# Kernel optimization log

Measured on AMD Instinct MI355X. Metric: run time of the kernel, lower is better.

## Reference

```python
import jax, jax.numpy as jnp
import numpy as np

B, C, H = 4, 64, 48
HEADS, BSWIN = 2, 4
BIG = [3, 6, 12, 24]      # big window edge per scale (cubic)
SMALL = [1, 2, 4, 8]      # small (pool) window edge per scale
NH = 3                    # small windows per big window per dim (= big/small)
L = NH ** 3               # tokens per big window after pooling
CPH = C // (HEADS * BSWIN)  # channels per head per scale = 8


def _rel_pos_index():
    coords = np.stack(np.meshgrid(*([np.arange(NH)] * 3), indexing='ij')).reshape(3, -1)
    rel = coords[:, :, None] - coords[:, None, :] + (NH - 1)
    span = 2 * NH - 1
    return jnp.asarray(rel[0] * span * span + rel[1] * span + rel[2])  # (L, L) int

REL_IDX = _rel_pos_index()


def _interp_matrix(n_in, n_out):
    # 1D linear interpolation matrix, align_corners=True (matches F.interpolate)
    if n_out == n_in:
        return jnp.eye(n_in, dtype=jnp.float32)
    pos = jnp.arange(n_out, dtype=jnp.float32) * (n_in - 1) / (n_out - 1)
    i0 = jnp.clip(jnp.floor(pos).astype(jnp.int32), 0, n_in - 2)
    w = pos - i0.astype(jnp.float32)
    r = jnp.arange(n_out)
    m = jnp.zeros((n_out, n_in), jnp.float32)
    return m.at[r, i0].add(1.0 - w).at[r, i0 + 1].add(w)


def _gather(x):
    # x: (B, C, H, H, H) -> (B, HEADS, sum_N, L, CPH)
    b = x.shape[0]
    x = x.reshape(b, BSWIN, HEADS, CPH, H, H, H)
    parts, Ns = [], []
    for i in range(BSWIN):
        bw, sw = BIG[i], SMALL[i]
        N1 = H // bw
        xi = x[:, i].reshape(b, HEADS, CPH, N1, NH, sw, N1, NH, sw, N1, NH, sw)
        xi = xi.max(axis=(5, 8, 11))  # max-pool each small window
        # (b, head, c, Nh, nh, Nw, nw, Nd, nd) -> b head (Nh Nw Nd) (nh nw nd) c
        xi = xi.transpose(0, 1, 3, 5, 7, 4, 6, 8, 2)
        parts.append(xi.reshape(b, HEADS, N1 ** 3, L, CPH))
        Ns.append(N1)
    return jnp.concatenate(parts, axis=2), Ns


def _scatter(attn, Ns):
    # attn: (B, HEADS, sum_N, L, CPH) -> (B, C, H, H, H)
    b = attn.shape[0]
    outs, idx = [], 0
    for i in range(BSWIN):
        bw, sw = BIG[i], SMALL[i]
        N1 = Ns[i]
        N = N1 ** 3
        o = attn[:, :, idx:idx + N].reshape(b, HEADS, N, NH, NH, NH, CPH)
        M = _interp_matrix(NH, bw)  # trilinear upsample by small window size
        o = jnp.einsum('bhnijkc,pi,qj,rk->bhnpqrc', o, M, M, M)
        o = o.reshape(b, HEADS, N1, N1, N1, bw, bw, bw, CPH)
        # b head Nh Nw Nd wh ww wd c -> b head c (Nh wh) (Nw ww) (Nd wd)
        o = o.transpose(0, 1, 8, 2, 5, 3, 6, 4, 7).reshape(b, HEADS, CPH, H, H, H)
        outs.append(o)
        idx += N
    out = jnp.stack(outs, axis=1)  # b bswin head c h w d
    return out.reshape(b, C, H, H, H)


def _attention(q, k, v, rpb_table):
    c = q.shape[-1]
    scores = jnp.einsum('bhNmc,bhNnc->bhNmn', q, k) / jnp.sqrt(jnp.asarray(c, q.dtype))
    w = jax.nn.softmax(scores, axis=-1)
    bias = rpb_table[REL_IDX].transpose(2, 0, 1)  # (head, L, L), added POST-softmax
    w = w + bias[None, :, None]
    return jnp.einsum('bhNmn,bhNnc->bhNmc', w, v)


def setup_inputs() -> dict:
    key = jax.random.key(0)
    kq, kk, kv, kp = jax.random.split(key, 4)
    shp = (B, C, H, H, H)
    return {
        'query': jax.random.normal(kq, shp, jnp.float32),
        'key': jax.random.normal(kk, shp, jnp.float32),
        'value': jax.random.normal(kv, shp, jnp.float32),
        'rpb_table': jax.random.normal(kp, ((2 * NH - 1) ** 3, HEADS), jnp.float32) * 0.02,
    }


def reference(query, key, value, rpb_table):
    q, Ns = _gather(query)
    k, _ = _gather(key)
    v, _ = _gather(value)
    attn = _attention(q, k, v, rpb_table)
    return _scatter(attn, Ns)
```

## Files before the change

kernel.cpp:

```cpp
#include <hip/hip_runtime.h>


static constexpr long S1 = 4L * 48 * 24 * 24 * 24;
static constexpr long S2 = 4L * 32 * 12 * 12 * 12;
static constexpr long S3 = 4L * 16 * 6 * 6 * 6;


__device__ __forceinline__ void pool48_body(int pid, float* xp,
                                            const float* __restrict__ q,
                                            const float* __restrict__ k,
                                            const float* __restrict__ v,
                                            float* __restrict__ P1)
{
    constexpr int RSTRIDE = 28;
    const int tz = pid % 3;
    int rest = pid / 3;
    const int zc = rest % 12; rest /= 12;
    const int c = rest % 48;
    const int b = rest / 48;

    const float* in = tz == 0 ? q : (tz == 1 ? k : v);
    float* o = P1 + (long)tz * S1;
    const float* base = in + ((long)b * 64 + 16 + c) * 110592 + (long)(zc * 4) * 2304;

    for (int i = threadIdx.x; i < 4 * 48 * 12; i += 256) {
        int p = i / 576;
        int rem = i % 576;
        int r = rem / 12;
        int x4 = rem % 12;
        float4 f = *(const float4*)(base + (long)p * 2304 + r * 48 + 4 * x4);
        float2 m = make_float2(fmaxf(f.x, f.y), fmaxf(f.z, f.w));
        *(float2*)(&xp[(p * 48 + r) * RSTRIDE + 2 * x4]) = m;
    }
    __syncthreads();

    for (int i = threadIdx.x; i < 288; i += 256) {
        int zl = i / 144;
        int rem = i % 144;
        int oy = rem / 6;
        int ox4 = rem % 6;
        const float* p0 = &xp[((2 * zl) * 48 + 2 * oy) * RSTRIDE + 4 * ox4];
        const float* p1 = p0 + RSTRIDE;
        const float* p2 = p0 + 48 * RSTRIDE;
        const float* p3 = p2 + RSTRIDE;
        float4 a = *(const float4*)p0;
        float4 bb = *(const float4*)p1;
        float4 cc = *(const float4*)p2;
        float4 d = *(const float4*)p3;
        float4 r4 = make_float4(fmaxf(fmaxf(a.x, bb.x), fmaxf(cc.x, d.x)),
                                fmaxf(fmaxf(a.y, bb.y), fmaxf(cc.y, d.y)),
                                fmaxf(fmaxf(a.z, bb.z), fmaxf(cc.z, d.z)),
                                fmaxf(fmaxf(a.w, bb.w), fmaxf(cc.w, d.w)));
        long oaddr = (((long)b * 48 + c) * 24 + (zc * 2 + zl)) * 576 + oy * 24 + 4 * ox4;
        *(float4*)(o + oaddr) = r4;
    }
}

__device__ __forceinline__ void attn0_body(int aid, float* smem,
                                           const float* __restrict__ qsrc,
                                           const float* __restrict__ ksrc,
                                           const float* __restrict__ vsrc,
                                           const float* __restrict__ rpb,
                                           float* __restrict__ out)
{
    const int half = aid & 1;
    int rest = aid >> 1;
    const int Wy = rest % 16; rest /= 16;
    const int Wz = rest % 16; rest /= 16;
    const int head = rest % 2;
    const int b = rest / 2;

    float* tile = smem;
    float* bias = smem + 5184;
    const int tid = threadIdx.x;

    for (int i = tid; i < 2 * 729; i += 256) {
        int h = i / 729;
        int mn = i % 729;
        int m = mn / 27, n = mn % 27;
        int mi = m / 9, mj = (m / 3) % 3, mk = m % 3;
        int ni = n / 9, nj = (n / 3) % 3, nk = n % 3;
        int ridx = (mi - ni + 2) * 25 + (mj - nj + 2) * 5 + (mk - nk + 2);
        bias[i] = rpb[ridx * 2 + h];
    }

    for (int i = tid; i < 1296; i += 256) {
        int seg = i / 6;
        int off = (i % 6) * 4;
        int tz = seg / 72;
        int rem = seg % 72;
        int cph = rem / 9;
        int rem2 = rem % 9;
        int zt = rem2 / 3;
        int r = rem2 % 3;
        const float* src = tz == 0 ? qsrc : (tz == 1 ? ksrc : vsrc);
        long addr = ((((long)b * 64 + head * 8 + cph) * 48 + 3 * Wz + zt) * 48
                     + 3 * Wy + r) * 48 + half * 24 + off;
        float4 f = *(const float4*)(src + addr);
        float vals[4] = {f.x, f.y, f.z, f.w};
#pragma unroll
        for (int j = 0; j < 4; j++) {
            int xl = off + j;
            int wxl = xl / 3, tk = xl % 3;
            int tok = zt * 9 + r * 3 + tk;
            tile[((wxl * 3 + tz) * 27 + tok) * 8 + cph] = vals[j];
        }
    }
    __syncthreads();

    const int wx = tid >> 5;
    const int lane = tid & 31;
    if (lane < 27) {
        const int m = lane;
        const float* tq = tile + (wx * 3 + 0) * 27 * 8;
        const float* tk = tile + (wx * 3 + 1) * 27 * 8;
        const float* tv = tile + (wx * 3 + 2) * 27 * 8;
        float qr[8];
#pragma unroll
        for (int c = 0; c < 8; c++) qr[c] = tq[m * 8 + c];

        float s[27];
        float mx = -1e30f;
#pragma unroll
        for (int n = 0; n < 27; n++) {
            float acc = 0.f;
#pragma unroll
            for (int c = 0; c < 8; c++) acc += qr[c] * tk[n * 8 + c];
            acc *= 0.35355339059327373f;
            s[n] = acc;
            mx = fmaxf(mx, acc);
        }
        float sum = 0.f;
#pragma unroll
        for (int n = 0; n < 27; n++) {
            s[n] = __expf(s[n] - mx);
            sum += s[n];
        }
        float rs = 1.0f / sum;

        float o[8] = {0, 0, 0, 0, 0, 0, 0, 0};
#pragma unroll
        for (int n = 0; n < 27; n++) {
            float wgt = s[n] * rs + bias[(head * 27 + m) * 27 + n];
#pragma unroll
            for (int c = 0; c < 8; c++) o[c] += wgt * tv[n * 8 + c];
        }
        float* to = tile + (wx * 3 + 0) * 27 * 8;
#pragma unroll
        for (int c = 0; c < 8; c++) to[m * 8 + c] = o[c];
    }
    __syncthreads();

    for (int i = tid; i < 432; i += 256) {
        int x4i = i % 6;
        int t2 = i / 6;
        int cph = t2 % 8; t2 /= 8;
        int y = t2 % 3;
        int zl = t2 / 3;
        float4 res;
        float* rr = (float*)&res;
#pragma unroll
        for (int e = 0; e < 4; e++) {
            int xl = x4i * 4 + e;
            int wxl = xl / 3, tk = xl % 3;
            int tok = zl * 9 + y * 3 + tk;
            rr[e] = tile[(wxl * 3 + 0) * 27 * 8 + tok * 8 + cph];
        }
        int z = 3 * Wz + zl;
        int Y = 3 * Wy + y;
        long oaddr = (((long)(b * 64 + head * 8 + cph) * 48 + z) * 48 + Y) * 48
                     + half * 24 + x4i * 4;
        *(float4*)(out + oaddr) = res;
    }
}

__global__ void fused_pool_attn0(const float* __restrict__ q,
                                 const float* __restrict__ k,
                                 const float* __restrict__ v,
                                 const float* __restrict__ rpb,
                                 float* __restrict__ P1,
                                 float* __restrict__ out)
{
    __shared__ float smem[6642];
    const int bx = blockIdx.x;
    if (bx < 8192 && (bx & 1) == 0) {
        attn0_body(bx >> 1, smem, q, k, v, rpb, out);
    } else {
        int pid = (bx < 8192) ? (bx >> 1) : (bx - 4096);
        pool48_body(pid, smem, q, k, v, P1);
    }
}

template <int OUTW>
__global__ void pool_kernel(const float* __restrict__ in0,
                            const float* __restrict__ in1,
                            const float* __restrict__ in2,
                            float* __restrict__ out, long outStride,
                            int Cin, int chOff, int Cout, int Din, int n)
{
    const float* in = blockIdx.y == 0 ? in0 : (blockIdx.y == 1 ? in1 : in2);
    float* o = out + (long)blockIdx.y * outStride;
    const int Dout = Din >> 1;
    const int QX = Dout / OUTW;
    int idx = blockIdx.x * blockDim.x + threadIdx.x;
    if (idx >= n) return;
    int qx = idx % QX;
    int t = idx / QX;
    int y = t % Dout; t /= Dout;
    int z = t % Dout; t /= Dout;
    int c = t % Cout;
    int b = t / Cout;
    const float* p = in + ((((long)b * Cin + c + chOff) * Din + 2 * z) * Din + 2 * y) * Din
                        + qx * (2 * OUTW);
    const float* rows[4] = { p, p + Din, p + (long)Din * Din, p + (long)Din * Din + Din };

    float v2[4][2 * OUTW];
#pragma unroll
    for (int r = 0; r < 4; r++) {
#pragma unroll
        for (int j = 0; j < OUTW / 2; j++) {
            float4 f = *(const float4*)(rows[r] + 4 * j);
            v2[r][4 * j + 0] = f.x; v2[r][4 * j + 1] = f.y;
            v2[r][4 * j + 2] = f.z; v2[r][4 * j + 3] = f.w;
        }
    }
    float res[OUTW];
#pragma unroll
    for (int i = 0; i < OUTW; i++) {
        float m0 = fmaxf(v2[0][2 * i], v2[0][2 * i + 1]);
        float m1 = fmaxf(v2[1][2 * i], v2[1][2 * i + 1]);
        float m2 = fmaxf(v2[2][2 * i], v2[2][2 * i + 1]);
        float m3 = fmaxf(v2[3][2 * i], v2[3][2 * i + 1]);
        res[i] = fmaxf(fmaxf(m0, m1), fmaxf(m2, m3));
    }
    long oaddr = ((((long)b * Cout + c) * Dout + z) * Dout + y) * Dout + qx * OUTW;
    if (OUTW == 4) {
        *(float4*)(o + oaddr) = make_float4(res[0], res[1], res[2], res[3 % OUTW]);
    } else {
        *(float2*)(o + oaddr) = make_float2(res[0], res[1]);
    }
}

template <int S>
__global__ void attn_kernel(const float* __restrict__ qsrc,
                            const float* __restrict__ ksrc,
                            const float* __restrict__ vsrc,
                            const float* __restrict__ rpb,
                            float* __restrict__ attnOut)
{
    constexpr int N1 = (S == 1 ? 8 : S == 2 ? 4 : 2);
    constexpr int D  = 3 * N1;
    constexpr int Cs = (S == 1 ? 48 : S == 2 ? 32 : 16);
    constexpr int scaleOff = (S == 1 ? 4096 : S == 2 ? 4608 : 4672);
    constexpr int VEC = (S == 3 ? 2 : 4);
    constexpr int SEG = 3 * D;
    constexpr int NSEG = 72;
    constexpr int TOTV = NSEG * SEG / VEC;

    __shared__ float tile[N1][3][27][8];
    __shared__ float bias_lds[2][27][27];

    const int b = blockIdx.z;
    const int head = blockIdx.y;
    const int Wz = blockIdx.x / N1;
    const int Wy = blockIdx.x % N1;

    for (int i = threadIdx.x; i < 2 * 729; i += blockDim.x) {
        int h = i / 729;
        int mn = i % 729;
        int m = mn / 27, n = mn % 27;
        int mi = m / 9, mj = (m / 3) % 3, mk = m % 3;
        int ni = n / 9, nj = (n / 3) % 3, nk = n % 3;
        int ridx = (mi - ni + 2) * 25 + (mj - nj + 2) * 5 + (mk - nk + 2);
        bias_lds[h][m][n] = rpb[ridx * 2 + h];
    }

    for (int i = threadIdx.x; i < TOTV; i += blockDim.x) {
        int seg = i / (SEG / VEC);
        int off = (i % (SEG / VEC)) * VEC;
        int tz = seg / 24;
        int rem = seg % 24;
        int cph = rem / 3;
        int zt = rem % 3;
        const float* src = tz == 0 ? qsrc : (tz == 1 ? ksrc : vsrc);
        long base = ((((long)b * Cs + head * 8 + cph) * D + (3 * Wz + zt)) * D + 3 * Wy) * (long)D;
        const float* sp = src + base + off;
        float vals[VEC];
        if (VEC == 4) {
            float4 f = *(const float4*)sp;
            vals[0] = f.x; vals[1] = f.y; vals[2] = f.z; vals[3 % VEC] = f.w;
        } else {
            float2 f = *(const float2*)sp;
            vals[0] = f.x; vals[1] = f.y;
        }
#pragma unroll
        for (int j = 0; j < VEC; j++) {
            int f = off + j;
            int r = f / D;
            int x = f % D;
            tile[x / 3][tz][zt * 9 + r * 3 + (x % 3)][cph] = vals[j];
        }
    }
    __syncthreads();

    const int wx = threadIdx.x >> 5;
    const int lane = threadIdx.x & 31;
    if (lane >= 27) return;
    const int m = lane;

    float qr[8];
#pragma unroll
    for (int c = 0; c < 8; c++) qr[c] = tile[wx][0][m][c];

    float s[27];
    float mx = -1e30f;
#pragma unroll
    for (int n = 0; n < 27; n++) {
        float acc = 0.f;
#pragma unroll
        for (int c = 0; c < 8; c++) acc += qr[c] * tile[wx][1][n][c];
        acc *= 0.35355339059327373f;
        s[n] = acc;
        mx = fmaxf(mx, acc);
    }
    float sum = 0.f;
#pragma unroll
    for (int n = 0; n < 27; n++) {
        s[n] = __expf(s[n] - mx);
        sum += s[n];
    }
    float rs = 1.0f / sum;

    float o[8] = {0, 0, 0, 0, 0, 0, 0, 0};
#pragma unroll
    for (int n = 0; n < 27; n++) {
        float wgt = s[n] * rs + bias_lds[head][m][n];
#pragma unroll
        for (int c = 0; c < 8; c++) o[c] += wgt * tile[wx][2][n][c];
    }

    const int win = (Wz * N1 + Wy) * N1 + wx;
    float* dst = attnOut + (((long)(b * 2 + head) * 4680 + scaleOff + win) * 27 + m) * 8;
    *(float4*)(dst) = make_float4(o[0], o[1], o[2], o[3]);
    *(float4*)(dst + 4) = make_float4(o[4], o[5], o[6], o[7]);
}

template <int S>
__device__ __forceinline__ void scatter_impl(const float* __restrict__ attn,
                                             float* __restrict__ out,
                                             float* lds, int t, int b, int head,
                                             int tid)
{
    constexpr int bw = (S == 1 ? 6 : S == 2 ? 12 : 24);
    constexpr int N1 = 48 / bw;
    constexpr int scaleOff = (S == 1 ? 4096 : S == 2 ? 4608 : 4672);
    constexpr int CZ = (S == 1 ? 3 : 1);
    constexpr int NZC = bw / CZ;
    constexpr int LDSF = N1 * 216;
    constexpr int NF4 = CZ * bw * 8 * 12;

    const int zc = t % NZC; t /= NZC;
    const int Wy = t % N1;
    const int Wz = t / N1;

    const float* src = attn + ((long)(b * 2 + head) * 4680 + scaleOff + (Wz * N1 + Wy) * N1) * 216;
    for (int i = tid; i < LDSF / 4; i += 256)
        *(float4*)(lds + 4 * i) = *(const float4*)(src + 4 * i);
    __syncthreads();

    const float inv = 2.0f / (float)(bw - 1);

    for (int i = tid; i < NF4; i += 256) {
        int x4 = i % 12;
        int t2 = i / 12;
        int cph = t2 % 8; t2 /= 8;
        int y = t2 % bw;
        int zl = t2 / bw;
        int wp = zc * CZ + zl;

        float posp = wp * inv; int i0p = min((int)posp, 1); float fp = posp - (float)i0p;
        float posq = y * inv;  int i0q = min((int)posq, 1); float fq = posq - (float)i0q;
        float wpv[2] = {1.f - fp, fp};
        float wqv[2] = {1.f - fq, fq};
        float4 res;
        float* rr = (float*)&res;
#pragma unroll
        for (int e = 0; e < 4; e++) {
            int r = x4 * 4 + e;
            int Wx = r / bw, wr = r % bw;
            float posr = wr * inv; int i0r = min((int)posr, 1); float fr = posr - (float)i0r;
            float wrv[2] = {1.f - fr, fr};
            const float* basep = lds + Wx * 216 + cph;
            float acc = 0.f;
#pragma unroll
            for (int di = 0; di < 2; di++) {
#pragma unroll
                for (int dj = 0; dj < 2; dj++) {
#pragma unroll
                    for (int dk = 0; dk < 2; dk++) {
                        int tok = ((i0p + di) * 3 + (i0q + dj)) * 3 + (i0r + dk);
                        acc += wpv[di] * wqv[dj] * wrv[dk] * basep[tok * 8];
                    }
                }
            }
            rr[e] = acc;
        }

        int z = Wz * bw + wp;
        int Y = Wy * bw + y;
        long oaddr = (((long)(b * 64 + S * 16 + head * 8 + cph) * 48 + z) * 48 + Y) * 48 + x4 * 4;
        *(float4*)(out + oaddr) = res;
    }
}

__global__ void scatter_all(const float* __restrict__ attn, float* __restrict__ out)
{
    __shared__ float lds[8 * 216];
    const int b = blockIdx.z;
    const int head = blockIdx.y;
    const int bx = blockIdx.x;
    const int tid = threadIdx.x;
    if (bx < 128)      scatter_impl<1>(attn, out, lds, bx,       b, head, tid);
    else if (bx < 320) scatter_impl<2>(attn, out, lds, bx - 128, b, head, tid);
    else               scatter_impl<3>(attn, out, lds, bx - 320, b, head, tid);
}

extern "C" void kernel_launch(void* const* d_in, const int* in_sizes, int n_in,
                              void* d_out, int out_size, void* d_ws, size_t ws_size,
                              hipStream_t stream)
{
    const float* q   = (const float*)d_in[0];
    const float* k   = (const float*)d_in[1];
    const float* v   = (const float*)d_in[2];
    const float* rpb = (const float*)d_in[3];
    float* out = (float*)d_out;

    float* ws = (float*)d_ws;
    float* P1 = ws;
    float* P2 = ws + 3 * S1;
    float* P3 = ws + 3 * S1 + 3 * S2;
    float* attn = ws + 3 * S1 + 3 * S2 + 3 * S3;

    fused_pool_attn0<<<11008, 256, 0, stream>>>(q, k, v, rpb, P1, out);

    {
        const int n2 = 4 * 32 * 12 * 12 * 3;
        dim3 g2((n2 + 255) / 256, 3);
        pool_kernel<4><<<g2, 256, 0, stream>>>(P1, P1 + S1, P1 + 2 * S1, P2, S2, 48, 16, 32, 24, n2);

        const int n3 = 4 * 16 * 6 * 6 * 3;
        dim3 g3((n3 + 255) / 256, 3);
        pool_kernel<2><<<g3, 256, 0, stream>>>(P2, P2 + S2, P2 + 2 * S2, P3, S3, 32, 16, 16, 12, n3);
    }

    attn_kernel<1><<<dim3(64, 2, 4), 256, 0, stream>>>(P1, P1 + S1, P1 + 2 * S1, rpb, attn);
    attn_kernel<2><<<dim3(16, 2, 4), 128, 0, stream>>>(P2, P2 + S2, P2 + 2 * S2, rpb, attn);
    attn_kernel<3><<<dim3(4, 2, 4), 64, 0, stream>>>(P3, P3 + S3, P3 + 2 * S3, rpb, attn);

    scatter_all<<<dim3(416, 2, 4), 256, 0, stream>>>(attn, out);
}
```

Measured before the change: 187.8 us.

## Fuse attention with upsample scatter, merge pool levels, use nontemporal loads

The scale-1 pooling now reads global memory directly with nontemporal loads instead of staging through LDS. The scale-2 and scale-3 pools are merged into one kernel that keeps the scale-2 result in shared memory. Attention for scales 1 and 2 is fused with the trilinear upsample, so output is written straight to the result without a round trip through an attention buffer. The LDS tile layout becomes channel-major with padding, and the bias table is loaded for only one head. The intent is fewer launches and less global traffic, at the cost of a more complex attention-scatter kernel and possibly lower parallelism in the fused kernels.

```diff
diff --git a/kernel.cpp b/kernel.cpp
--- a/kernel.cpp
+++ b/kernel.cpp
@@ -5,54 +5,56 @@
 static constexpr long S2 = 4L * 32 * 12 * 12 * 12;
 static constexpr long S3 = 4L * 16 * 6 * 6 * 6;
 
-
-__device__ __forceinline__ void pool48_body(int pid, float* xp,
-                                            const float* __restrict__ q,
-                                            const float* __restrict__ k,
-                                            const float* __restrict__ v,
-                                            float* __restrict__ P1)
-{
-    constexpr int RSTRIDE = 28;
+typedef float f4 __attribute__((ext_vector_type(4)));
+
+__device__ __forceinline__ f4 ntload(const float* p) {
+    return __builtin_nontemporal_load((const f4*)p);
+}
+__device__ __forceinline__ void ntstore(float* p, f4 v) {
+    __builtin_nontemporal_store(v, (f4*)p);
+}
+__device__ __forceinline__ f4 vmax(f4 a, f4 b) {
+    f4 r;
+    r[0] = fmaxf(a[0], b[0]); r[1] = fmaxf(a[1], b[1]);
+    r[2] = fmaxf(a[2], b[2]); r[3] = fmaxf(a[3], b[3]);
+    return r;
+}
+
+__device__ __forceinline__ void pool1_body(int pid,
+                                           const float* __restrict__ q,
+                                           const float* __restrict__ k,
+                                           const float* __restrict__ v,
+                                           float* __restrict__ P1)
+{
     const int tz = pid % 3;
     int rest = pid / 3;
     const int zc = rest % 12; rest /= 12;
     const int c = rest % 48;
     const int b = rest / 48;
-
     const float* in = tz == 0 ? q : (tz == 1 ? k : v);
     float* o = P1 + (long)tz * S1;
-    const float* base = in + ((long)b * 64 + 16 + c) * 110592 + (long)(zc * 4) * 2304;
-
-    for (int i = threadIdx.x; i < 4 * 48 * 12; i += 256) {
-        int p = i / 576;
-        int rem = i % 576;
-        int r = rem / 12;
-        int x4 = rem % 12;
-        float4 f = *(const float4*)(base + (long)p * 2304 + r * 48 + 4 * x4);
-        float2 m = make_float2(fmaxf(f.x, f.y), fmaxf(f.z, f.w));
-        *(float2*)(&xp[(p * 48 + r) * RSTRIDE + 2 * x4]) = m;
-    }
-    __syncthreads();
+    const float* base = in + ((long)b * 64 + 16 + c) * 110592;
 
     for (int i = threadIdx.x; i < 288; i += 256) {
-        int zl = i / 144;
-        int rem = i % 144;
-        int oy = rem / 6;
-        int ox4 = rem % 6;
-        const float* p0 = &xp[((2 * zl) * 48 + 2 * oy) * RSTRIDE + 4 * ox4];
-        const float* p1 = p0 + RSTRIDE;
-        const float* p2 = p0 + 48 * RSTRIDE;
-        const float* p3 = p2 + RSTRIDE;
-        float4 a = *(const float4*)p0;
-        float4 bb = *(const float4*)p1;
-        float4 cc = *(const float4*)p2;
-        float4 d = *(const float4*)p3;
-        float4 r4 = make_float4(fmaxf(fmaxf(a.x, bb.x), fmaxf(cc.x, d.x)),
-                                fmaxf(fmaxf(a.y, bb.y), fmaxf(cc.y, d.y)),
-                                fmaxf(fmaxf(a.z, bb.z), fmaxf(cc.z, d.z)),
-                                fmaxf(fmaxf(a.w, bb.w), fmaxf(cc.w, d.w)));
-        long oaddr = (((long)b * 48 + c) * 24 + (zc * 2 + zl)) * 576 + oy * 24 + 4 * ox4;
-        *(float4*)(o + oaddr) = r4;
+        const int zl = i / 144;
+        const int rem = i % 144;
+        const int oy = rem / 6;
+        const int qx = rem % 6;
+        const int oz = zc * 2 + zl;
+        const float* p = base + ((long)(2 * oz) * 48 + 2 * oy) * 48 + qx * 8;
+        f4 r0a = ntload(p),        r0b = ntload(p + 4);
+        f4 r1a = ntload(p + 48),   r1b = ntload(p + 52);
+        f4 r2a = ntload(p + 2304), r2b = ntload(p + 2308);
+        f4 r3a = ntload(p + 2352), r3b = ntload(p + 2356);
+        f4 ma = vmax(vmax(r0a, r1a), vmax(r2a, r3a));
+        f4 mb = vmax(vmax(r0b, r1b), vmax(r2b, r3b));
+        f4 res;
+        res[0] = fmaxf(ma[0], ma[1]);
+        res[1] = fmaxf(ma[2], ma[3]);
+        res[2] = fmaxf(mb[0], mb[1]);
+        res[3] = fmaxf(mb[2], mb[3]);
+        long oaddr = (((long)b * 48 + c) * 24 + oz) * 576 + oy * 24 + qx * 4;
+        *(f4*)(o + oaddr) = res;
     }
 }
 
@@ -63,25 +65,22 @@
                                            const float* __restrict__ rpb,
                                            float* __restrict__ out)
 {
-    const int half = aid & 1;
-    int rest = aid >> 1;
+    float* tile = smem;
+    float* bias = smem + 5376;
+    const int tid = threadIdx.x;
+    int rest = aid;
+    const int half = rest & 1; rest >>= 1;
     const int Wy = rest % 16; rest /= 16;
     const int Wz = rest % 16; rest /= 16;
     const int head = rest % 2;
     const int b = rest / 2;
 
-    float* tile = smem;
-    float* bias = smem + 5184;
-    const int tid = threadIdx.x;
-
-    for (int i = tid; i < 2 * 729; i += 256) {
-        int h = i / 729;
-        int mn = i % 729;
-        int m = mn / 27, n = mn % 27;
+    for (int i = tid; i < 729; i += 256) {
+        int m = i / 27, n = i % 27;
         int mi = m / 9, mj = (m / 3) % 3, mk = m % 3;
         int ni = n / 9, nj = (n / 3) % 3, nk = n % 3;
         int ridx = (mi - ni + 2) * 25 + (mj - nj + 2) * 5 + (mk - nk + 2);
-        bias[i] = rpb[ridx * 2 + h];
+        bias[i] = rpb[ridx * 2 + head];
     }
 
     for (int i = tid; i < 1296; i += 256) {
@@ -96,14 +95,13 @@
         const float* src = tz == 0 ? qsrc : (tz == 1 ? ksrc : vsrc);
         long addr = ((((long)b * 64 + head * 8 + cph) * 48 + 3 * Wz + zt) * 48
                      + 3 * Wy + r) * 48 + half * 24 + off;
-        float4 f = *(const float4*)(src + addr);
-        float vals[4] = {f.x, f.y, f.z, f.w};
+        f4 f = ntload(src + addr);
 #pragma unroll
         for (int j = 0; j < 4; j++) {
             int xl = off + j;
-            int wxl = xl / 3, tk = xl % 3;
+            int wxl = xl / 3, tk = xl - wxl * 3;
             int tok = zt * 9 + r * 3 + tk;
-            tile[((wxl * 3 + tz) * 27 + tok) * 8 + cph] = vals[j];
+            tile[((wxl * 3 + tz) * 8 + cph) * 28 + tok] = f[j];
         }
     }
     __syncthreads();
@@ -112,12 +110,12 @@
     const int lane = tid & 31;
     if (lane < 27) {
         const int m = lane;
-        const float* tq = tile + (wx * 3 + 0) * 27 * 8;
-        const float* tk = tile + (wx * 3 + 1) * 27 * 8;
-        const float* tv = tile + (wx * 3 + 2) * 27 * 8;
+        float* b0 = tile + wx * 672;
+        const float* kb = b0 + 224;
+        const float* vb = b0 + 448;
         float qr[8];
 #pragma unroll
-        for (int c = 0; c < 8; c++) qr[c] = tq[m * 8 + c];
+        for (int c = 0; c < 8; c++) qr[c] = b0[c * 28 + m];
 
         float s[27];
         float mx = -1e30f;
@@ -125,7 +123,7 @@
         for (int n = 0; n < 27; n++) {
             float acc = 0.f;
 #pragma unroll
-            for (int c = 0; c < 8; c++) acc += qr[c] * tk[n * 8 + c];
+            for (int c = 0; c < 8; c++) acc += qr[c] * kb[c * 28 + n];
             acc *= 0.35355339059327373f;
             s[n] = acc;
             mx = fmaxf(mx, acc);
@@ -137,17 +135,15 @@
             sum += s[n];
         }
         float rs = 1.0f / sum;
-
         float o[8] = {0, 0, 0, 0, 0, 0, 0, 0};
 #pragma unroll
         for (int n = 0; n < 27; n++) {
-            float wgt = s[n] * rs + bias[(head * 27 + m) * 27 + n];
-#pragma unroll
-            for (int c = 0; c < 8; c++) o[c] += wgt * tv[n * 8 + c];
-        }
-        float* to = tile + (wx * 3 + 0) * 27 * 8;
-#pragma unroll
-        for (int c = 0; c < 8; c++) to[m * 8 + c] = o[c];
+            float w = s[n] * rs + bias[m * 27 + n];
+#pragma unroll
+            for (int c = 0; c < 8; c++) o[c] += w * vb[c * 28 + n];
+        }
+#pragma unroll
+        for (int c = 0; c < 8; c++) b0[c * 28 + m] = o[c];
     }
     __syncthreads();
 
@@ -157,161 +153,265 @@
         int cph = t2 % 8; t2 /= 8;
         int y = t2 % 3;
         int zl = t2 / 3;
-        float4 res;
-        float* rr = (float*)&res;
+        f4 res;
 #pragma unroll
         for (int e = 0; e < 4; e++) {
             int xl = x4i * 4 + e;
-            int wxl = xl / 3, tk = xl % 3;
+            int wxl = xl / 3, tk = xl - wxl * 3;
             int tok = zl * 9 + y * 3 + tk;
-            rr[e] = tile[(wxl * 3 + 0) * 27 * 8 + tok * 8 + cph];
+            res[e] = tile[wxl * 672 + cph * 28 + tok];
         }
         int z = 3 * Wz + zl;
         int Y = 3 * Wy + y;
         long oaddr = (((long)(b * 64 + head * 8 + cph) * 48 + z) * 48 + Y) * 48
                      + half * 24 + x4i * 4;
-        *(float4*)(out + oaddr) = res;
-    }
-}
-
-__global__ void fused_pool_attn0(const float* __restrict__ q,
-                                 const float* __restrict__ k,
-                                 const float* __restrict__ v,
-                                 const float* __restrict__ rpb,
-                                 float* __restrict__ P1,
-                                 float* __restrict__ out)
-{
-    __shared__ float smem[6642];
+        ntstore(out + oaddr, res);
+    }
+}
+
+__global__ void fused_k1(const float* __restrict__ q, const float* __restrict__ k,
+                         const float* __restrict__ v, const float* __restrict__ rpb,
+                         float* __restrict__ P1, float* __restrict__ out)
+{
+    __shared__ __align__(16) float smem[6105];
     const int bx = blockIdx.x;
     if (bx < 8192 && (bx & 1) == 0) {
         attn0_body(bx >> 1, smem, q, k, v, rpb, out);
     } else {
         int pid = (bx < 8192) ? (bx >> 1) : (bx - 4096);
-        pool48_body(pid, smem, q, k, v, P1);
-    }
-}
-
-template <int OUTW>
-__global__ void pool_kernel(const float* __restrict__ in0,
-                            const float* __restrict__ in1,
-                            const float* __restrict__ in2,
-                            float* __restrict__ out, long outStride,
-                            int Cin, int chOff, int Cout, int Din, int n)
-{
-    const float* in = blockIdx.y == 0 ? in0 : (blockIdx.y == 1 ? in1 : in2);
-    float* o = out + (long)blockIdx.y * outStride;
-    const int Dout = Din >> 1;
-    const int QX = Dout / OUTW;
-    int idx = blockIdx.x * blockDim.x + threadIdx.x;
-    if (idx >= n) return;
-    int qx = idx % QX;
-    int t = idx / QX;
-    int y = t % Dout; t /= Dout;
-    int z = t % Dout; t /= Dout;
-    int c = t % Cout;
-    int b = t / Cout;
-    const float* p = in + ((((long)b * Cin + c + chOff) * Din + 2 * z) * Din + 2 * y) * Din
-                        + qx * (2 * OUTW);
-    const float* rows[4] = { p, p + Din, p + (long)Din * Din, p + (long)Din * Din + Din };
-
-    float v2[4][2 * OUTW];
-#pragma unroll
-    for (int r = 0; r < 4; r++) {
-#pragma unroll
-        for (int j = 0; j < OUTW / 2; j++) {
-            float4 f = *(const float4*)(rows[r] + 4 * j);
-            v2[r][4 * j + 0] = f.x; v2[r][4 * j + 1] = f.y;
-            v2[r][4 * j + 2] = f.z; v2[r][4 * j + 3] = f.w;
-        }
-    }
-    float res[OUTW];
-#pragma unroll
-    for (int i = 0; i < OUTW; i++) {
-        float m0 = fmaxf(v2[0][2 * i], v2[0][2 * i + 1]);
-        float m1 = fmaxf(v2[1][2 * i], v2[1][2 * i + 1]);
-        float m2 = fmaxf(v2[2][2 * i], v2[2][2 * i + 1]);
-        float m3 = fmaxf(v2[3][2 * i], v2[3][2 * i + 1]);
-        res[i] = fmaxf(fmaxf(m0, m1), fmaxf(m2, m3));
-    }
-    long oaddr = ((((long)b * Cout + c) * Dout + z) * Dout + y) * Dout + qx * OUTW;
-    if (OUTW == 4) {
-        *(float4*)(o + oaddr) = make_float4(res[0], res[1], res[2], res[3 % OUTW]);
-    } else {
-        *(float2*)(o + oaddr) = make_float2(res[0], res[1]);
+        pool1_body(pid, q, k, v, P1);
+    }
+}
+
+__global__ void pool23_kernel(const float* __restrict__ P1,
+                              float* __restrict__ P2, float* __restrict__ P3)
+{
+    __shared__ __align__(16) float vol[13824];
+    __shared__ __align__(16) float p2b[1728];
+    int bx = blockIdx.x;
+    const int c2 = bx % 32; bx /= 32;
+    const int b = bx % 4;
+    const int tz = bx / 4;
+    const float* src = P1 + (long)tz * S1 + ((long)b * 48 + c2 + 16) * 13824;
+    for (int i = threadIdx.x; i < 3456; i += 256)
+        *(f4*)(vol + 4 * i) = *(const f4*)(src + 4 * i);
+    __syncthreads();
+
+    float* o2 = P2 + (long)tz * S2 + ((long)b * 32 + c2) * 1728;
+    for (int i = threadIdx.x; i < 432; i += 256) {
+        const int x4 = i % 3;
+        const int t = i / 3;
+        const int y = t % 12;
+        const int z = t / 12;
+        const float* p0 = vol + (2 * z * 24 + 2 * y) * 24 + x4 * 8;
+        f4 res;
+#pragma unroll
+        for (int e = 0; e < 4; e++) {
+            float m0 = fmaxf(p0[2 * e], p0[2 * e + 1]);
+            float m1 = fmaxf(p0[24 + 2 * e], p0[24 + 2 * e + 1]);
+            float m2 = fmaxf(p0[576 + 2 * e], p0[576 + 2 * e + 1]);
+            float m3 = fmaxf(p0[600 + 2 * e], p0[600 + 2 * e + 1]);
+            res[e] = fmaxf(fmaxf(m0, m1), fmaxf(m2, m3));
+        }
+        const int oidx = (z * 12 + y) * 12 + x4 * 4;
+        *(f4*)(o2 + oidx) = res;
+        *(f4*)(p2b + oidx) = res;
+    }
+    __syncthreads();
+
+    if (c2 >= 16) {
+        float* o3 = P3 + (long)tz * S3 + ((long)b * 16 + (c2 - 16)) * 216;
+        for (int i = threadIdx.x; i < 108; i += 256) {
+            const int x2 = i % 3;
+            const int t = i / 3;
+            const int y = t % 6;
+            const int z = t / 6;
+            const float* p0 = p2b + (2 * z * 12 + 2 * y) * 12 + x2 * 4;
+            float r0 = fmaxf(fmaxf(p0[0], p0[1]), fmaxf(p0[12], p0[13]));
+            float r1 = fmaxf(fmaxf(p0[144], p0[145]), fmaxf(p0[156], p0[157]));
+            float s0 = fmaxf(fmaxf(p0[2], p0[3]), fmaxf(p0[14], p0[15]));
+            float s1 = fmaxf(fmaxf(p0[146], p0[147]), fmaxf(p0[158], p0[159]));
+            float2 res = make_float2(fmaxf(r0, r1), fmaxf(s0, s1));
+            *(float2*)(o3 + (z * 6 + y) * 6 + x2 * 2) = res;
+        }
     }
 }
 
 template <int S>
-__global__ void attn_kernel(const float* __restrict__ qsrc,
-                            const float* __restrict__ ksrc,
-                            const float* __restrict__ vsrc,
-                            const float* __restrict__ rpb,
-                            float* __restrict__ attnOut)
-{
-    constexpr int N1 = (S == 1 ? 8 : S == 2 ? 4 : 2);
-    constexpr int D  = 3 * N1;
-    constexpr int Cs = (S == 1 ? 48 : S == 2 ? 32 : 16);
-    constexpr int scaleOff = (S == 1 ? 4096 : S == 2 ? 4608 : 4672);
-    constexpr int VEC = (S == 3 ? 2 : 4);
-    constexpr int SEG = 3 * D;
-    constexpr int NSEG = 72;
-    constexpr int TOTV = NSEG * SEG / VEC;
-
-    __shared__ float tile[N1][3][27][8];
-    __shared__ float bias_lds[2][27][27];
-
-    const int b = blockIdx.z;
-    const int head = blockIdx.y;
-    const int Wz = blockIdx.x / N1;
-    const int Wy = blockIdx.x % N1;
-
-    for (int i = threadIdx.x; i < 2 * 729; i += blockDim.x) {
-        int h = i / 729;
-        int mn = i % 729;
-        int m = mn / 27, n = mn % 27;
+__global__ void attn_sc_kernel(const float* __restrict__ qsrc,
+                               const float* __restrict__ ksrc,
+                               const float* __restrict__ vsrc,
+                               const float* __restrict__ rpb,
+                               float* __restrict__ out)
+{
+    constexpr int N1 = (S == 1 ? 8 : 4);
+    constexpr int D = 3 * N1;
+    constexpr int bw = 48 / N1;
+    constexpr int Cs = (S == 1 ? 48 : 32);
+    constexpr int SEGF4 = 3 * D / 4;
+    __shared__ float tile[N1 * 672];
+    __shared__ float bias[729];
+    const int b = blockIdx.z, head = blockIdx.y;
+    const int Wz = blockIdx.x / N1, Wy = blockIdx.x % N1;
+    const int tid = threadIdx.x;
+
+    for (int i = tid; i < 729; i += 256) {
+        int m = i / 27, n = i % 27;
         int mi = m / 9, mj = (m / 3) % 3, mk = m % 3;
         int ni = n / 9, nj = (n / 3) % 3, nk = n % 3;
         int ridx = (mi - ni + 2) * 25 + (mj - nj + 2) * 5 + (mk - nk + 2);
-        bias_lds[h][m][n] = rpb[ridx * 2 + h];
-    }
-
-    for (int i = threadIdx.x; i < TOTV; i += blockDim.x) {
-        int seg = i / (SEG / VEC);
-        int off = (i % (SEG / VEC)) * VEC;
+        bias[i] = rpb[ridx * 2 + head];
+    }
+
+    for (int i = tid; i < 72 * SEGF4; i += 256) {
+        int seg = i / SEGF4;
+        int off = (i % SEGF4) * 4;
         int tz = seg / 24;
         int rem = seg % 24;
         int cph = rem / 3;
         int zt = rem % 3;
         const float* src = tz == 0 ? qsrc : (tz == 1 ? ksrc : vsrc);
-        long base = ((((long)b * Cs + head * 8 + cph) * D + (3 * Wz + zt)) * D + 3 * Wy) * (long)D;
-        const float* sp = src + base + off;
-        float vals[VEC];
-        if (VEC == 4) {
-            float4 f = *(const float4*)sp;
-            vals[0] = f.x; vals[1] = f.y; vals[2] = f.z; vals[3 % VEC] = f.w;
-        } else {
-            float2 f = *(const float2*)sp;
-            vals[0] = f.x; vals[1] = f.y;
-        }
-#pragma unroll
-        for (int j = 0; j < VEC; j++) {
-            int f = off + j;
-            int r = f / D;
-            int x = f % D;
+        long base = ((((long)b * Cs + head * 8 + cph) * D + 3 * Wz + zt) * D + 3 * Wy) * (long)D;
+        float4 f = *(const float4*)(src + base + off);
+        float vals[4] = {f.x, f.y, f.z, f.w};
+#pragma unroll
+        for (int j = 0; j < 4; j++) {
+            int xl = off + j;
+            int r = xl / D;
+            int x = xl - r * D;
+            int wxl = x / 3, tk = x - wxl * 3;
+            tile[((wxl * 3 + tz) * 8 + cph) * 28 + zt * 9 + r * 3 + tk] = vals[j];
+        }
+    }
+    __syncthreads();
+
+    const int wx = tid >> 5;
+    const int lane = tid & 31;
+    if (wx < N1 && lane < 27) {
+        const int m = lane;
+        float* b0 = tile + wx * 672;
+        const float* kb = b0 + 224;
+        const float* vb = b0 + 448;
+        float qr[8];
+#pragma unroll
+        for (int c = 0; c < 8; c++) qr[c] = b0[c * 28 + m];
+        float s[27];
+        float mx = -1e30f;
+#pragma unroll
+        for (int n = 0; n < 27; n++) {
+            float acc = 0.f;
+#pragma unroll
+            for (int c = 0; c < 8; c++) acc += qr[c] * kb[c * 28 + n];
+            acc *= 0.35355339059327373f;
+            s[n] = acc;
+            mx = fmaxf(mx, acc);
+        }
+        float sum = 0.f;
+#pragma unroll
+        for (int n = 0; n < 27; n++) {
+            s[n] = __expf(s[n] - mx);
+            sum += s[n];
+        }
+        float rs = 1.0f / sum;
+        float o[8] = {0, 0, 0, 0, 0, 0, 0, 0};
+#pragma unroll
+        for (int n = 0; n < 27; n++) {
+            float w = s[n] * rs + bias[m * 27 + n];
+#pragma unroll
+            for (int c = 0; c < 8; c++) o[c] += w * vb[c * 28 + n];
+        }
+#pragma unroll
+        for (int c = 0; c < 8; c++) b0[c * 28 + m] = o[c];
+    }
+    __syncthreads();
+
+    constexpr int NF4 = bw * bw * 96;
+    const float inv = 2.0f / (float)(bw - 1);
+    for (int i = tid; i < NF4; i += 256) {
+        int x4 = i % 12;
+        int t2 = i / 12;
+        int cph = t2 % 8; t2 /= 8;
+        int wq = t2 % bw;
+        int wp = t2 / bw;
+        float posp = wp * inv; int i0p = min((int)posp, 1); float fp = posp - (float)i0p;
+        float posq = wq * inv; int i0q = min((int)posq, 1); float fq = posq - (float)i0q;
+        float wpv[2] = {1.f - fp, fp};
+        float wqv[2] = {1.f - fq, fq};
+        f4 res;
+#pragma unroll
+        for (int e = 0; e < 4; e++) {
+            int xg = x4 * 4 + e;
+            int Wx = xg / bw, wr = xg - Wx * bw;
+            float posr = wr * inv; int i0r = min((int)posr, 1); float fr = posr - (float)i0r;
+            float wrv[2] = {1.f - fr, fr};
+            const float* bp = tile + Wx * 672 + cph * 28;
+            float acc = 0.f;
+#pragma unroll
+            for (int di = 0; di < 2; di++) {
+#pragma unroll
+                for (int dj = 0; dj < 2; dj++) {
+#pragma unroll
+                    for (int dk = 0; dk < 2; dk++) {
+                        int tok = ((i0p + di) * 3 + (i0q + dj)) * 3 + (i0r + dk);
+                        acc += wpv[di] * wqv[dj] * wrv[dk] * bp[tok];
+                    }
+                }
+            }
+            res[e] = acc;
+        }
+        long oaddr = (((long)(b * 64 + S * 16 + head * 8 + cph) * 48 + Wz * bw + wp) * 48
+                      + Wy * bw + wq) * 48 + x4 * 4;
+        ntstore(out + oaddr, res);
+    }
+}
+
+__global__ void attn3_kernel(const float* __restrict__ qsrc,
+                             const float* __restrict__ ksrc,
+                             const float* __restrict__ vsrc,
+                             const float* __restrict__ rpb,
+                             float* __restrict__ attnOut)
+{
+    __shared__ float tile[2][3][27][8];
+    __shared__ float bias[729];
+    const int b = blockIdx.z, head = blockIdx.y;
+    const int Wz = blockIdx.x / 2, Wy = blockIdx.x % 2;
+    const int tid = threadIdx.x;
+
+    for (int i = tid; i < 729; i += 64) {
+        int m = i / 27, n = i % 27;
+        int mi = m / 9, mj = (m / 3) % 3, mk = m % 3;
+        int ni = n / 9, nj = (n / 3) % 3, nk = n % 3;
+        int ridx = (mi - ni + 2) * 25 + (mj - nj + 2) * 5 + (mk - nk + 2);
+        bias[i] = rpb[ridx * 2 + head];
+    }
+    for (int i = tid; i < 648; i += 64) {
+        int seg = i / 9;
+        int off = (i % 9) * 2;
+        int tz = seg / 24;
+        int rem = seg % 24;
+        int cph = rem / 3;
+        int zt = rem % 3;
+        const float* src = tz == 0 ? qsrc : (tz == 1 ? ksrc : vsrc);
+        long base = ((((long)b * 16 + head * 8 + cph) * 6 + 3 * Wz + zt) * 6 + 3 * Wy) * 6L;
+        float2 f = *(const float2*)(src + base + off);
+        float vals[2] = {f.x, f.y};
+#pragma unroll
+        for (int j = 0; j < 2; j++) {
+            int xl = off + j;
+            int r = xl / 6;
+            int x = xl - r * 6;
             tile[x / 3][tz][zt * 9 + r * 3 + (x % 3)][cph] = vals[j];
         }
     }
     __syncthreads();
 
-    const int wx = threadIdx.x >> 5;
-    const int lane = threadIdx.x & 31;
+    const int wx = tid >> 5;
+    const int lane = tid & 31;
     if (lane >= 27) return;
     const int m = lane;
-
     float qr[8];
 #pragma unroll
     for (int c = 0; c < 8; c++) qr[c] = tile[wx][0][m][c];
-
     float s[27];
     float mx = -1e30f;
 #pragma unroll
@@ -330,64 +430,48 @@
         sum += s[n];
     }
     float rs = 1.0f / sum;
-
     float o[8] = {0, 0, 0, 0, 0, 0, 0, 0};
 #pragma unroll
     for (int n = 0; n < 27; n++) {
-        float wgt = s[n] * rs + bias_lds[head][m][n];
-#pragma unroll
-        for (int c = 0; c < 8; c++) o[c] += wgt * tile[wx][2][n][c];
-    }
-
-    const int win = (Wz * N1 + Wy) * N1 + wx;
-    float* dst = attnOut + (((long)(b * 2 + head) * 4680 + scaleOff + win) * 27 + m) * 8;
+        float w = s[n] * rs + bias[m * 27 + n];
+#pragma unroll
+        for (int c = 0; c < 8; c++) o[c] += w * tile[wx][2][n][c];
+    }
+    const int win = (Wz * 2 + Wy) * 2 + wx;
+    float* dst = attnOut + (((long)(b * 2 + head) * 4680 + 4672 + win) * 27 + m) * 8;
     *(float4*)(dst) = make_float4(o[0], o[1], o[2], o[3]);
     *(float4*)(dst + 4) = make_float4(o[4], o[5], o[6], o[7]);
 }
 
-template <int S>
-__device__ __forceinline__ void scatter_impl(const float* __restrict__ attn,
-                                             float* __restrict__ out,
-                                             float* lds, int t, int b, int head,
-                                             int tid)
-{
-    constexpr int bw = (S == 1 ? 6 : S == 2 ? 12 : 24);
-    constexpr int N1 = 48 / bw;
-    constexpr int scaleOff = (S == 1 ? 4096 : S == 2 ? 4608 : 4672);
-    constexpr int CZ = (S == 1 ? 3 : 1);
-    constexpr int NZC = bw / CZ;
-    constexpr int LDSF = N1 * 216;
-    constexpr int NF4 = CZ * bw * 8 * 12;
-
-    const int zc = t % NZC; t /= NZC;
-    const int Wy = t % N1;
-    const int Wz = t / N1;
-
-    const float* src = attn + ((long)(b * 2 + head) * 4680 + scaleOff + (Wz * N1 + Wy) * N1) * 216;
-    for (int i = tid; i < LDSF / 4; i += 256)
-        *(float4*)(lds + 4 * i) = *(const float4*)(src + 4 * i);
-    __syncthreads();
-
-    const float inv = 2.0f / (float)(bw - 1);
-
-    for (int i = tid; i < NF4; i += 256) {
+__global__ void scatter3_kernel(const float* __restrict__ attn, float* __restrict__ out)
+{
+    __shared__ __align__(16) float lds[432];
+    const int b = blockIdx.z, head = blockIdx.y;
+    int t = blockIdx.x;
+    const int zc = t % 24; t /= 24;
+    const int Wy = t % 2;
+    const int Wz = t / 2;
+    const float* src = attn + ((long)(b * 2 + head) * 4680 + 4672 + (Wz * 2 + Wy) * 2) * 216;
+    for (int i = threadIdx.x; i < 108; i += 256)
+        *(f4*)(lds + 4 * i) = *(const f4*)(src + 4 * i);
+    __syncthreads();
+
+    const float inv = 2.0f / 23.0f;
+    for (int i = threadIdx.x; i < 2304; i += 256) {
         int x4 = i % 12;
         int t2 = i / 12;
-        int cph = t2 % 8; t2 /= 8;
-        int y = t2 % bw;
-        int zl = t2 / bw;
-        int wp = zc * CZ + zl;
-
+        int cph = t2 % 8;
+        int y = t2 / 8;
+        int wp = zc;
         float posp = wp * inv; int i0p = min((int)posp, 1); float fp = posp - (float)i0p;
         float posq = y * inv;  int i0q = min((int)posq, 1); float fq = posq - (float)i0q;
         float wpv[2] = {1.f - fp, fp};
         float wqv[2] = {1.f - fq, fq};
-        float4 res;
-        float* rr = (float*)&res;
+        f4 res;
 #pragma unroll
         for (int e = 0; e < 4; e++) {
             int r = x4 * 4 + e;
-            int Wx = r / bw, wr = r % bw;
+            int Wx = r / 24, wr = r % 24;
             float posr = wr * inv; int i0r = min((int)posr, 1); float fr = posr - (float)i0r;
             float wrv[2] = {1.f - fr, fr};
             const float* basep = lds + Wx * 216 + cph;
@@ -403,26 +487,13 @@
                     }
                 }
             }
-            rr[e] = acc;
-        }
-
-        int z = Wz * bw + wp;
-        int Y = Wy * bw + y;
-        long oaddr = (((long)(b * 64 + S * 16 + head * 8 + cph) * 48 + z) * 48 + Y) * 48 + x4 * 4;
-        *(float4*)(out + oaddr) = res;
-    }
-}
-
-__global__ void scatter_all(const float* __restrict__ attn, float* __restrict__ out)
-{
-    __shared__ float lds[8 * 216];
-    const int b = blockIdx.z;
-    const int head = blockIdx.y;
-    const int bx = blockIdx.x;
-    const int tid = threadIdx.x;
-    if (bx < 128)      scatter_impl<1>(attn, out, lds, bx,       b, head, tid);
-    else if (bx < 320) scatter_impl<2>(attn, out, lds, bx - 128, b, head, tid);
-    else               scatter_impl<3>(attn, out, lds, bx - 320, b, head, tid);
+            res[e] = acc;
+        }
+        int z = Wz * 24 + wp;
+        int Y = Wy * 24 + y;
+        long oaddr = (((long)(b * 64 + 48 + head * 8 + cph) * 48 + z) * 48 + Y) * 48 + x4 * 4;
+        ntstore(out + oaddr, res);
+    }
 }
 
 extern "C" void kernel_launch(void* const* d_in, const int* in_sizes, int n_in,
@@ -441,21 +512,13 @@
     float* P3 = ws + 3 * S1 + 3 * S2;
     float* attn = ws + 3 * S1 + 3 * S2 + 3 * S3;
 
-    fused_pool_attn0<<<11008, 256, 0, stream>>>(q, k, v, rpb, P1, out);
-
-    {
-        const int n2 = 4 * 32 * 12 * 12 * 3;
-        dim3 g2((n2 + 255) / 256, 3);
-        pool_kernel<4><<<g2, 256, 0, stream>>>(P1, P1 + S1, P1 + 2 * S1, P2, S2, 48, 16, 32, 24, n2);
-
-        const int n3 = 4 * 16 * 6 * 6 * 3;
-        dim3 g3((n3 + 255) / 256, 3);
-        pool_kernel<2><<<g3, 256, 0, stream>>>(P2, P2 + S2, P2 + 2 * S2, P3, S3, 32, 16, 16, 12, n3);
-    }
-
-    attn_kernel<1><<<dim3(64, 2, 4), 256, 0, stream>>>(P1, P1 + S1, P1 + 2 * S1, rpb, attn);
-    attn_kernel<2><<<dim3(16, 2, 4), 128, 0, stream>>>(P2, P2 + S2, P2 + 2 * S2, rpb, attn);
-    attn_kernel<3><<<dim3(4, 2, 4), 64, 0, stream>>>(P3, P3 + S3, P3 + 2 * S3, rpb, attn);
-
-    scatter_all<<<dim3(416, 2, 4), 256, 0, stream>>>(attn, out);
-}
+    fused_k1<<<11008, 256, 0, stream>>>(q, k, v, rpb, P1, out);
+
+    pool23_kernel<<<384, 256, 0, stream>>>(P1, P2, P3);
+
+    attn_sc_kernel<1><<<dim3(64, 2, 4), 256, 0, stream>>>(P1, P1 + S1, P1 + 2 * S1, rpb, out);
+    attn_sc_kernel<2><<<dim3(16, 2, 4), 256, 0, stream>>>(P2, P2 + S2, P2 + 2 * S2, rpb, out);
+
+    attn3_kernel<<<dim3(4, 2, 4), 64, 0, stream>>>(P3, P3 + S3, P3 + 2 * S3, rpb, attn);
+    scatter3_kernel<<<dim3(96, 2, 4), 256, 0, stream>>>(attn, out);
+}
```

Result: slower. 216.7 us (+15.4%).
